# Optimization experiments

Hardware: AMD Instinct MI355X
Metric: run time of the kernel (lower is better)

## Reference

```python
import jax, jax.numpy as jnp
import numpy as np

NUM_FEAT = 10

def _flatten(x):
    # [B,T,C,H,W] -> [B,C,T*H*W]
    B, T, C, H, W = x.shape
    return jnp.transpose(x, (0, 2, 1, 3, 4)).reshape(B, C, T * H * W)

def _conv1x1(w, b, x):
    # pointwise Conv1d: w [F,C], b [F], x [B,C,N] -> [B,F,N]
    return jnp.einsum('fc,bcn->bfn', w, x) + b[None, :, None]

def setup_inputs() -> dict:
    key = jax.random.key(0)
    ks = jax.random.split(key, 9)
    B, T, C, H, W = 1, 5, 64, 32, 32
    F = NUM_FEAT
    return {
        'input1': jax.random.normal(ks[0], (B, T, C, H, W), jnp.float32),
        'input2': jax.random.normal(ks[1], (B, T, C, H, W), jnp.float32),
        'act_weights': jax.random.uniform(ks[2], (3,), jnp.float32),
        'conv1_w': jax.random.normal(ks[3], (F, C), jnp.float32) * 0.05,
        'conv1_b': jnp.zeros((F,), jnp.float32),
        'conv2_w': jax.random.normal(ks[4], (F, C), jnp.float32) * 0.05,
        'conv2_b': jnp.zeros((F,), jnp.float32),
        'g3_w': jax.random.normal(ks[5], (F, C), jnp.float32) * 0.05,
        'g3_b': jnp.zeros((F,), jnp.float32),
    }

def reference(input1, input2, act_weights, conv1_w, conv1_b, conv2_w, conv2_b, g3_w, g3_b):
    B, T, C, H, W = input1.shape
    F = conv1_w.shape[0]
    x1 = _flatten(input1)                    # [B,C,N]
    x2 = _flatten(input2)                    # [B,C,N]
    q = _conv1x1(conv1_w, conv1_b, x1)       # [B,F,N]
    k = _conv1x1(conv2_w, conv2_b, x2)       # [B,F,N]
    v = _conv1x1(g3_w, g3_b, x1)             # [B,F,N]
    scores = jnp.einsum('bfn,bfm->bnm', q, k)  # [B,N,N] (same math, computed once)

    def branch(act_scores):
        o = jnp.einsum('bnm,bfm->bnf', act_scores, v)      # [B,N,F]
        o = o.reshape(B, T, H, W, F)
        return jnp.transpose(o, (0, 1, 4, 2, 3))           # [B,T,F,H,W]

    out = act_weights[0] * branch(jax.nn.relu(scores))
    out = out + act_weights[1] * branch(jax.nn.sigmoid(scores))
    # NOTE: original code scales the softmax branch by act_weights[0] (bug kept faithfully)
    out = out + act_weights[0] * branch(jax.nn.softmax(scores, axis=1))
    return out
```

## Files before the change

kernel.cpp:

```cpp
#include <hip/hip_runtime.h>

#define N_TOK   5120
#define C_IN    64
#define F_OUT   10
#define FP      12

#define DTILE   40
#define MTILE   40
#define NCHUNKS 128
#define MCHUNKS 128

__global__ __launch_bounds__(256) void qkv_kernel(
    const float* __restrict__ x1, const float* __restrict__ x2,
    const float* __restrict__ w1, const float* __restrict__ b1,
    const float* __restrict__ w2, const float* __restrict__ b2,
    const float* __restrict__ w3, const float* __restrict__ b3,
    float* __restrict__ Q, float* __restrict__ K, float* __restrict__ V,
    float* __restrict__ out, float* __restrict__ dsum)
{
    if (blockIdx.x < 200)
        out[blockIdx.x * 256 + threadIdx.x] = 0.f;
    else if (blockIdx.x < 220)
        dsum[(blockIdx.x - 200) * 256 + threadIdx.x] = 0.f;

    int arr = blockIdx.x / 200;
    int rem = blockIdx.x - arr * 200;
    int f   = rem / 20;
    int nbk = rem - f * 20;
    int n   = nbk * 256 + threadIdx.x;
    int t = n >> 10, p = n & 1023;

    const float* x    = (arr == 1) ? x2 : x1;
    const float* w    = (arr == 0) ? w1 : (arr == 1) ? w2 : w3;
    const float* bias = (arr == 0) ? b1 : (arr == 1) ? b2 : b3;
    float*       dst  = (arr == 0) ? Q  : (arr == 1) ? K  : V;

    const float* xp = x + t * (C_IN * 1024) + p;
    const float* wr = w + f * C_IN;

    float4 wv[16];
#pragma unroll
    for (int i = 0; i < 16; ++i) wv[i] = ((const float4*)wr)[i];

    float acc = 0.f;
#pragma unroll
    for (int i = 0; i < 16; ++i) {
        acc = fmaf(wv[i].x, xp[(4 * i + 0) * 1024], acc);
        acc = fmaf(wv[i].y, xp[(4 * i + 1) * 1024], acc);
        acc = fmaf(wv[i].z, xp[(4 * i + 2) * 1024], acc);
        acc = fmaf(wv[i].w, xp[(4 * i + 3) * 1024], acc);
    }
    dst[n * FP + f] = acc + bias[f];
}

__global__ __launch_bounds__(256) void denom_kernel(
    const float* __restrict__ Q, const float* __restrict__ K,
    float* __restrict__ dsum, int nclen)
{
    int mTile = blockIdx.x % 5;
    int nc    = blockIdx.x / 5;
    int tid   = threadIdx.x;
    int m0 = mTile * 1024 + tid;

    float kk[4][10];
#pragma unroll
    for (int c = 0; c < 4; ++c) {
        const float* kp = K + (m0 + c * 256) * FP;
        float4 a = ((const float4*)kp)[0];
        float4 b = ((const float4*)kp)[1];
        float2 e = ((const float2*)kp)[4];
        kk[c][0]=a.x; kk[c][1]=a.y; kk[c][2]=a.z; kk[c][3]=a.w;
        kk[c][4]=b.x; kk[c][5]=b.y; kk[c][6]=b.z; kk[c][7]=b.w;
        kk[c][8]=e.x; kk[c][9]=e.y;
    }

    __shared__ __align__(16) float sq[DTILE * FP];

    float d[4] = {0.f, 0.f, 0.f, 0.f};
    int n0 = nc * nclen;
    for (int base = n0; base < n0 + nclen; base += DTILE) {
        __syncthreads();
        if (tid < DTILE * FP / 4)
            ((float4*)sq)[tid] = ((const float4*)(Q + base * FP))[tid];
        __syncthreads();
#pragma unroll 2
        for (int j = 0; j < DTILE; ++j) {
            const float4* qp = (const float4*)(sq + j * FP);
            float4 qa = qp[0], qb = qp[1], qc = qp[2];
            float qq[10] = {qa.x, qa.y, qa.z, qa.w, qb.x, qb.y, qb.z, qb.w,
                            qc.x, qc.y};
#pragma unroll
            for (int c = 0; c < 4; ++c) {
                float s = 0.f;
#pragma unroll
                for (int f = 0; f < F_OUT; ++f) s = fmaf(qq[f], kk[c][f], s);
                d[c] += __expf(fminf(s, 60.f));
            }
        }
    }
#pragma unroll
    for (int c = 0; c < 4; ++c) atomicAdd(&dsum[m0 + c * 256], d[c]);
}

__global__ __launch_bounds__(256) void main_kernel(
    const float* __restrict__ Q, const float* __restrict__ K,
    const float* __restrict__ V, const float* __restrict__ dsum,
    const float* __restrict__ aw, float* __restrict__ out, int mclen)
{
    int nTile = blockIdx.x % 4;
    int mc    = blockIdx.x / 4;
    int tid   = threadIdx.x;
    int nb = nTile * 1280 + tid;
    float w0 = aw[0], w1v = aw[1];

    float q[5][10];
#pragma unroll
    for (int r = 0; r < 5; ++r) {
        const float* qp = Q + (nb + r * 256) * FP;
        float4 a = ((const float4*)qp)[0];
        float4 b = ((const float4*)qp)[1];
        float2 e = ((const float2*)qp)[4];
        q[r][0]=a.x; q[r][1]=a.y; q[r][2]=a.z; q[r][3]=a.w;
        q[r][4]=b.x; q[r][5]=b.y; q[r][6]=b.z; q[r][7]=b.w;
        q[r][8]=e.x; q[r][9]=e.y;
    }

    float acc[5][F_OUT];
#pragma unroll
    for (int r = 0; r < 5; ++r)
#pragma unroll
        for (int f = 0; f < F_OUT; ++f) acc[r][f] = 0.f;

    __shared__ __align__(16) float sk[MTILE * FP];
    __shared__ __align__(16) float sv[MTILE * FP];
    __shared__ float siw[MTILE];

    int mstart = mc * mclen;
    for (int mbase = mstart; mbase < mstart + mclen; mbase += MTILE) {
        __syncthreads();
        if (tid < 120)
            ((float4*)sk)[tid] = ((const float4*)(K + mbase * FP))[tid];
        else if (tid < 240)
            ((float4*)sv)[tid - 120] = ((const float4*)(V + mbase * FP))[tid - 120];
        if (tid < MTILE)
            siw[tid] = w0 / dsum[mbase + tid];
        __syncthreads();

#pragma unroll 2
        for (int j = 0; j < MTILE; ++j) {
            const float4* kp = (const float4*)(sk + j * FP);
            float4 ka = kp[0], kb = kp[1], kc = kp[2];
            float kk[10] = {ka.x, ka.y, ka.z, ka.w, kb.x, kb.y, kb.z, kb.w,
                            kc.x, kc.y};
            float iw = siw[j];
            const float4* vp = (const float4*)(sv + j * FP);
            float4 va = vp[0], vb = vp[1], vc = vp[2];
            float vv[10] = {va.x, va.y, va.z, va.w, vb.x, vb.y, vb.z, vb.w,
                            vc.x, vc.y};

#pragma unroll
            for (int r = 0; r < 5; ++r) {
                float s = 0.f;
#pragma unroll
                for (int f = 0; f < F_OUT; ++f) s = fmaf(q[r][f], kk[f], s);
                float rl = fmaxf(s, 0.f);
                float e  = __expf(fminf(s, 60.f));
                float sg = e * __builtin_amdgcn_rcpf(1.f + e);
                float cf = fmaf(e, iw, fmaf(w1v, sg, w0 * rl));
#pragma unroll
                for (int f = 0; f < F_OUT; ++f) acc[r][f] = fmaf(cf, vv[f], acc[r][f]);
            }
        }
    }

#pragma unroll
    for (int r = 0; r < 5; ++r) {
        int n = nb + r * 256;
        int t = n >> 10, p = n & 1023;
        float* obase = out + ((t * F_OUT) << 10) + p;
#pragma unroll
        for (int f = 0; f < F_OUT; ++f)
            atomicAdd(obase + (f << 10), acc[r][f]);
    }
}

extern "C" void kernel_launch(void* const* d_in, const int* in_sizes, int n_in,
                              void* d_out, int out_size, void* d_ws, size_t ws_size,
                              hipStream_t stream)
{
    const float* in1 = (const float*)d_in[0];
    const float* in2 = (const float*)d_in[1];
    const float* aw  = (const float*)d_in[2];
    const float* w1  = (const float*)d_in[3];
    const float* b1  = (const float*)d_in[4];
    const float* w2  = (const float*)d_in[5];
    const float* b2  = (const float*)d_in[6];
    const float* w3  = (const float*)d_in[7];
    const float* b3  = (const float*)d_in[8];
    float* out = (float*)d_out;

    float* ws   = (float*)d_ws;
    float* Q    = ws;
    float* K    = Q + N_TOK * FP;
    float* V    = K + N_TOK * FP;
    float* dsum = V + N_TOK * FP;

    int nclen = N_TOK / NCHUNKS;
    int mclen = N_TOK / MCHUNKS;

    qkv_kernel<<<600, 256, 0, stream>>>(in1, in2, w1, b1, w2, b2, w3, b3,
                                        Q, K, V, out, dsum);
    denom_kernel<<<5 * NCHUNKS, 256, 0, stream>>>(Q, K, dsum, nclen);
    main_kernel<<<4 * MCHUNKS, 256, 0, stream>>>(Q, K, V, dsum, aw, out, mclen);
}
```

Baseline: 130.1 us.

## Fuse QKV, denominator and main passes into one persistent kernel with grid barriers

Merges the three launches into a single kernel of 1024 blocks, separated by two software grid barriers built on atomic counters, with a memset to reset the counters. Each block now handles one tile of 20 tokens in the denominator and main phases, replacing the chunked loops. The 10-term dot products are split into two independent FMA chains to shorten dependency latency. This removes kernel launch gaps and tail effects, but the barrier assumes all 1024 blocks are resident at once, which relies on the launch_bounds occupancy hint. It also adds spin-wait costs and more atomics into out and dsum.

```diff
diff --git a/kernel.cpp b/kernel.cpp
--- a/kernel.cpp
+++ b/kernel.cpp
@@ -5,164 +5,176 @@
 #define F_OUT   10
 #define FP      12
 
-#define DTILE   40
-#define MTILE   40
-#define NCHUNKS 128
-#define MCHUNKS 128
-
-__global__ __launch_bounds__(256) void qkv_kernel(
+#define GRID    1024
+#define TILE    20
+
+__device__ __forceinline__ void grid_barrier(unsigned* cnt, unsigned nblk)
+{
+    __syncthreads();
+    if (threadIdx.x == 0) {
+        __threadfence();
+        atomicAdd(cnt, 1u);
+        while (__hip_atomic_load(cnt, __ATOMIC_RELAXED,
+                                 __HIP_MEMORY_SCOPE_AGENT) < nblk)
+            __builtin_amdgcn_s_sleep(2);
+        __threadfence();
+    }
+    __syncthreads();
+}
+
+__global__ __launch_bounds__(256, 4) void fused_kernel(
     const float* __restrict__ x1, const float* __restrict__ x2,
+    const float* __restrict__ aw,
     const float* __restrict__ w1, const float* __restrict__ b1,
     const float* __restrict__ w2, const float* __restrict__ b2,
     const float* __restrict__ w3, const float* __restrict__ b3,
     float* __restrict__ Q, float* __restrict__ K, float* __restrict__ V,
-    float* __restrict__ out, float* __restrict__ dsum)
+    float* __restrict__ dsum, float* __restrict__ out, unsigned* __restrict__ bar)
 {
-    if (blockIdx.x < 200)
-        out[blockIdx.x * 256 + threadIdx.x] = 0.f;
-    else if (blockIdx.x < 220)
-        dsum[(blockIdx.x - 200) * 256 + threadIdx.x] = 0.f;
-
-    int arr = blockIdx.x / 200;
-    int rem = blockIdx.x - arr * 200;
-    int f   = rem / 20;
-    int nbk = rem - f * 20;
-    int n   = nbk * 256 + threadIdx.x;
-    int t = n >> 10, p = n & 1023;
-
-    const float* x    = (arr == 1) ? x2 : x1;
-    const float* w    = (arr == 0) ? w1 : (arr == 1) ? w2 : w3;
-    const float* bias = (arr == 0) ? b1 : (arr == 1) ? b2 : b3;
-    float*       dst  = (arr == 0) ? Q  : (arr == 1) ? K  : V;
-
-    const float* xp = x + t * (C_IN * 1024) + p;
-    const float* wr = w + f * C_IN;
-
-    float4 wv[16];
-#pragma unroll
-    for (int i = 0; i < 16; ++i) wv[i] = ((const float4*)wr)[i];
-
-    float acc = 0.f;
-#pragma unroll
-    for (int i = 0; i < 16; ++i) {
-        acc = fmaf(wv[i].x, xp[(4 * i + 0) * 1024], acc);
-        acc = fmaf(wv[i].y, xp[(4 * i + 1) * 1024], acc);
-        acc = fmaf(wv[i].z, xp[(4 * i + 2) * 1024], acc);
-        acc = fmaf(wv[i].w, xp[(4 * i + 3) * 1024], acc);
-    }
-    dst[n * FP + f] = acc + bias[f];
-}
-
-__global__ __launch_bounds__(256) void denom_kernel(
-    const float* __restrict__ Q, const float* __restrict__ K,
-    float* __restrict__ dsum, int nclen)
-{
-    int mTile = blockIdx.x % 5;
-    int nc    = blockIdx.x / 5;
-    int tid   = threadIdx.x;
-    int m0 = mTile * 1024 + tid;
-
-    float kk[4][10];
-#pragma unroll
-    for (int c = 0; c < 4; ++c) {
-        const float* kp = K + (m0 + c * 256) * FP;
-        float4 a = ((const float4*)kp)[0];
-        float4 b = ((const float4*)kp)[1];
-        float2 e = ((const float2*)kp)[4];
-        kk[c][0]=a.x; kk[c][1]=a.y; kk[c][2]=a.z; kk[c][3]=a.w;
-        kk[c][4]=b.x; kk[c][5]=b.y; kk[c][6]=b.z; kk[c][7]=b.w;
-        kk[c][8]=e.x; kk[c][9]=e.y;
-    }
-
-    __shared__ __align__(16) float sq[DTILE * FP];
-
-    float d[4] = {0.f, 0.f, 0.f, 0.f};
-    int n0 = nc * nclen;
-    for (int base = n0; base < n0 + nclen; base += DTILE) {
+    const int vb  = blockIdx.x;
+    const int tid = threadIdx.x;
+
+    __shared__ __align__(16) float sq[TILE * FP];
+    __shared__ __align__(16) float sk[TILE * FP];
+    __shared__ __align__(16) float sv[TILE * FP];
+    __shared__ float siw[TILE];
+
+    if (vb < 600) {
+        int arr = vb / 200;
+        int rem = vb - arr * 200;
+        int f   = rem / 20;
+        int nbk = rem - f * 20;
+        int n   = nbk * 256 + tid;
+        int t = n >> 10, p = n & 1023;
+
+        const float* x    = (arr == 1) ? x2 : x1;
+        const float* w    = (arr == 0) ? w1 : (arr == 1) ? w2 : w3;
+        const float* bias = (arr == 0) ? b1 : (arr == 1) ? b2 : b3;
+        float*       dst  = (arr == 0) ? Q  : (arr == 1) ? K  : V;
+
+        const float* xp = x + t * (C_IN * 1024) + p;
+        const float* wr = w + f * C_IN;
+
+        float4 wv[16];
+#pragma unroll
+        for (int i = 0; i < 16; ++i) wv[i] = ((const float4*)wr)[i];
+
+        float acc = 0.f;
+#pragma unroll
+        for (int i = 0; i < 16; ++i) {
+            acc = fmaf(wv[i].x, xp[(4 * i + 0) * 1024], acc);
+            acc = fmaf(wv[i].y, xp[(4 * i + 1) * 1024], acc);
+            acc = fmaf(wv[i].z, xp[(4 * i + 2) * 1024], acc);
+            acc = fmaf(wv[i].w, xp[(4 * i + 3) * 1024], acc);
+        }
+        dst[n * FP + f] = acc + bias[f];
+    } else {
+        int z = (vb - 600) * 256 + tid;
+        if (z < 51200)       out[z] = 0.f;
+        else if (z < 56320)  dsum[z - 51200] = 0.f;
+    }
+
+    grid_barrier(bar, GRID);
+
+    {
+        int mTile = vb & 3;
+        int nc    = vb >> 2;
+        int m0 = mTile * 1280 + tid;
+
+        float kk[5][10];
+#pragma unroll
+        for (int c = 0; c < 5; ++c) {
+            const float* kp = K + (m0 + c * 256) * FP;
+            float4 a = ((const float4*)kp)[0];
+            float4 b = ((const float4*)kp)[1];
+            float2 e = ((const float2*)kp)[4];
+            kk[c][0]=a.x; kk[c][1]=a.y; kk[c][2]=a.z; kk[c][3]=a.w;
+            kk[c][4]=b.x; kk[c][5]=b.y; kk[c][6]=b.z; kk[c][7]=b.w;
+            kk[c][8]=e.x; kk[c][9]=e.y;
+        }
+
+        if (tid < TILE * FP / 4)
+            ((float4*)sq)[tid] = ((const float4*)(Q + nc * TILE * FP))[tid];
         __syncthreads();
-        if (tid < DTILE * FP / 4)
-            ((float4*)sq)[tid] = ((const float4*)(Q + base * FP))[tid];
-        __syncthreads();
+
+        float d[5] = {0.f, 0.f, 0.f, 0.f, 0.f};
 #pragma unroll 2
-        for (int j = 0; j < DTILE; ++j) {
+        for (int j = 0; j < TILE; ++j) {
             const float4* qp = (const float4*)(sq + j * FP);
             float4 qa = qp[0], qb = qp[1], qc = qp[2];
             float qq[10] = {qa.x, qa.y, qa.z, qa.w, qb.x, qb.y, qb.z, qb.w,
                             qc.x, qc.y};
 #pragma unroll
-            for (int c = 0; c < 4; ++c) {
-                float s = 0.f;
-#pragma unroll
-                for (int f = 0; f < F_OUT; ++f) s = fmaf(qq[f], kk[c][f], s);
-                d[c] += __expf(fminf(s, 60.f));
+            for (int c = 0; c < 5; ++c) {
+                float s0 = 0.f, s1 = 0.f;
+#pragma unroll
+                for (int f = 0; f < 5; ++f) {
+                    s0 = fmaf(qq[f],     kk[c][f],     s0);
+                    s1 = fmaf(qq[f + 5], kk[c][f + 5], s1);
+                }
+                d[c] += __expf(fminf(s0 + s1, 60.f));
             }
         }
-    }
-#pragma unroll
-    for (int c = 0; c < 4; ++c) atomicAdd(&dsum[m0 + c * 256], d[c]);
-}
-
-__global__ __launch_bounds__(256) void main_kernel(
-    const float* __restrict__ Q, const float* __restrict__ K,
-    const float* __restrict__ V, const float* __restrict__ dsum,
-    const float* __restrict__ aw, float* __restrict__ out, int mclen)
-{
-    int nTile = blockIdx.x % 4;
-    int mc    = blockIdx.x / 4;
-    int tid   = threadIdx.x;
-    int nb = nTile * 1280 + tid;
-    float w0 = aw[0], w1v = aw[1];
-
-    float q[5][10];
-#pragma unroll
-    for (int r = 0; r < 5; ++r) {
-        const float* qp = Q + (nb + r * 256) * FP;
-        float4 a = ((const float4*)qp)[0];
-        float4 b = ((const float4*)qp)[1];
-        float2 e = ((const float2*)qp)[4];
-        q[r][0]=a.x; q[r][1]=a.y; q[r][2]=a.z; q[r][3]=a.w;
-        q[r][4]=b.x; q[r][5]=b.y; q[r][6]=b.z; q[r][7]=b.w;
-        q[r][8]=e.x; q[r][9]=e.y;
-    }
-
-    float acc[5][F_OUT];
-#pragma unroll
-    for (int r = 0; r < 5; ++r)
-#pragma unroll
-        for (int f = 0; f < F_OUT; ++f) acc[r][f] = 0.f;
-
-    __shared__ __align__(16) float sk[MTILE * FP];
-    __shared__ __align__(16) float sv[MTILE * FP];
-    __shared__ float siw[MTILE];
-
-    int mstart = mc * mclen;
-    for (int mbase = mstart; mbase < mstart + mclen; mbase += MTILE) {
+#pragma unroll
+        for (int c = 0; c < 5; ++c) atomicAdd(&dsum[m0 + c * 256], d[c]);
+    }
+
+    grid_barrier(bar + 1, GRID);
+
+    {
+        int nTile = vb & 3;
+        int mc    = vb >> 2;
+        int nb = nTile * 1280 + tid;
+        int m0 = mc * TILE;
+        float w0 = aw[0], w1v = aw[1];
+
+        float q[5][10];
+#pragma unroll
+        for (int r = 0; r < 5; ++r) {
+            const float* qp = Q + (nb + r * 256) * FP;
+            float4 a = ((const float4*)qp)[0];
+            float4 b = ((const float4*)qp)[1];
+            float2 e = ((const float2*)qp)[4];
+            q[r][0]=a.x; q[r][1]=a.y; q[r][2]=a.z; q[r][3]=a.w;
+            q[r][4]=b.x; q[r][5]=b.y; q[r][6]=b.z; q[r][7]=b.w;
+            q[r][8]=e.x; q[r][9]=e.y;
+        }
+
+        if (tid < 60)
+            ((float4*)sk)[tid] = ((const float4*)(K + m0 * FP))[tid];
+        else if (tid >= 64 && tid < 124)
+            ((float4*)sv)[tid - 64] = ((const float4*)(V + m0 * FP))[tid - 64];
+        else if (tid >= 128 && tid < 128 + TILE)
+            siw[tid - 128] = w0 / dsum[m0 + tid - 128];
         __syncthreads();
-        if (tid < 120)
-            ((float4*)sk)[tid] = ((const float4*)(K + mbase * FP))[tid];
-        else if (tid < 240)
-            ((float4*)sv)[tid - 120] = ((const float4*)(V + mbase * FP))[tid - 120];
-        if (tid < MTILE)
-            siw[tid] = w0 / dsum[mbase + tid];
-        __syncthreads();
+
+        float acc[5][F_OUT];
+#pragma unroll
+        for (int r = 0; r < 5; ++r)
+#pragma unroll
+            for (int f = 0; f < F_OUT; ++f) acc[r][f] = 0.f;
 
 #pragma unroll 2
-        for (int j = 0; j < MTILE; ++j) {
+        for (int j = 0; j < TILE; ++j) {
             const float4* kp = (const float4*)(sk + j * FP);
             float4 ka = kp[0], kb = kp[1], kc = kp[2];
             float kk[10] = {ka.x, ka.y, ka.z, ka.w, kb.x, kb.y, kb.z, kb.w,
                             kc.x, kc.y};
             float iw = siw[j];
             const float4* vp = (const float4*)(sv + j * FP);
-            float4 va = vp[0], vb = vp[1], vc = vp[2];
-            float vv[10] = {va.x, va.y, va.z, va.w, vb.x, vb.y, vb.z, vb.w,
+            float4 va = vp[0], vb4 = vp[1], vc = vp[2];
+            float vv[10] = {va.x, va.y, va.z, va.w, vb4.x, vb4.y, vb4.z, vb4.w,
                             vc.x, vc.y};
 
 #pragma unroll
             for (int r = 0; r < 5; ++r) {
-                float s = 0.f;
-#pragma unroll
-                for (int f = 0; f < F_OUT; ++f) s = fmaf(q[r][f], kk[f], s);
+                float s0 = 0.f, s1 = 0.f;
+#pragma unroll
+                for (int f = 0; f < 5; ++f) {
+                    s0 = fmaf(q[r][f],     kk[f],     s0);
+                    s1 = fmaf(q[r][f + 5], kk[f + 5], s1);
+                }
+                float s  = s0 + s1;
                 float rl = fmaxf(s, 0.f);
                 float e  = __expf(fminf(s, 60.f));
                 float sg = e * __builtin_amdgcn_rcpf(1.f + e);
@@ -171,16 +183,16 @@
                 for (int f = 0; f < F_OUT; ++f) acc[r][f] = fmaf(cf, vv[f], acc[r][f]);
             }
         }
-    }
-
-#pragma unroll
-    for (int r = 0; r < 5; ++r) {
-        int n = nb + r * 256;
-        int t = n >> 10, p = n & 1023;
-        float* obase = out + ((t * F_OUT) << 10) + p;
-#pragma unroll
-        for (int f = 0; f < F_OUT; ++f)
-            atomicAdd(obase + (f << 10), acc[r][f]);
+
+#pragma unroll
+        for (int r = 0; r < 5; ++r) {
+            int n = nb + r * 256;
+            int t = n >> 10, p = n & 1023;
+            float* obase = out + ((t * F_OUT) << 10) + p;
+#pragma unroll
+            for (int f = 0; f < F_OUT; ++f)
+                atomicAdd(obase + (f << 10), acc[r][f]);
+        }
     }
 }
 
@@ -204,12 +216,9 @@
     float* K    = Q + N_TOK * FP;
     float* V    = K + N_TOK * FP;
     float* dsum = V + N_TOK * FP;
-
-    int nclen = N_TOK / NCHUNKS;
-    int mclen = N_TOK / MCHUNKS;
-
-    qkv_kernel<<<600, 256, 0, stream>>>(in1, in2, w1, b1, w2, b2, w3, b3,
-                                        Q, K, V, out, dsum);
-    denom_kernel<<<5 * NCHUNKS, 256, 0, stream>>>(Q, K, dsum, nclen);
-    main_kernel<<<4 * MCHUNKS, 256, 0, stream>>>(Q, K, V, dsum, aw, out, mclen);
+    unsigned* bar = (unsigned*)(dsum + N_TOK + 64);
+
+    hipMemsetAsync(bar, 0, 2 * sizeof(unsigned), stream);
+    fused_kernel<<<GRID, 256, 0, stream>>>(in1, in2, aw, w1, b1, w2, b2, w3, b3,
+                                           Q, K, V, dsum, out, bar);
 }
```

Measured after the change: 356.1 us. 174% more time.
